# Optimization experiments

Measured on AMD Instinct MI355X. Metric: run time of the kernel, lower is better.

Reference implementation:

```python
import jax, jax.numpy as jnp
import numpy as np

NUM_REL = 20000
NUM_EDGES = 640000
DIM_IN = 128
DIM_OUT = 128
NUM_HEAD = 8
DIM_HID = DIM_OUT // NUM_HEAD
NUM_BIN = 10
NEG_SLOPE = 0.2


def leaky_relu(x):
    return jnp.where(x >= 0, x, NEG_SLOPE * x)


def setup_inputs() -> dict:
    key = jax.random.key(0)
    ks = jax.random.split(key, 8)
    emb_rel = jax.random.normal(ks[0], (NUM_REL, DIM_IN), dtype=jnp.float32)
    head = jax.random.randint(ks[1], (NUM_EDGES, 1), 0, NUM_REL)
    tail = jax.random.randint(ks[2], (NUM_EDGES, 1), 0, NUM_REL)
    bins = jax.random.randint(ks[3], (NUM_EDGES, 1), 0, NUM_BIN)
    relation_triplets = jnp.concatenate([head, tail, bins], axis=-1).astype(jnp.int64)
    # xavier-normal-ish init
    attn_proj_w = jax.random.normal(ks[4], (DIM_OUT, 2 * DIM_IN), dtype=jnp.float32) * (2.0 / np.sqrt(2 * DIM_IN + DIM_OUT))
    attn_proj_b = jnp.zeros((DIM_OUT,), dtype=jnp.float32)
    attn_bin = jax.random.normal(ks[5], (NUM_BIN, NUM_HEAD, 1), dtype=jnp.float32) * 0.3
    attn_vec = jax.random.normal(ks[6], (1, NUM_HEAD, DIM_HID), dtype=jnp.float32) * (2.0 / np.sqrt(NUM_HEAD * DIM_HID))
    aggr_proj_w = jax.random.normal(ks[7], (DIM_OUT, DIM_IN), dtype=jnp.float32) * (2.0 / np.sqrt(DIM_IN + DIM_OUT))
    aggr_proj_b = jnp.zeros((DIM_OUT,), dtype=jnp.float32)
    return {"emb_rel": emb_rel, "relation_triplets": relation_triplets,
            "attn_proj_w": attn_proj_w, "attn_proj_b": attn_proj_b,
            "attn_bin": attn_bin, "attn_vec": attn_vec,
            "aggr_proj_w": aggr_proj_w, "aggr_proj_b": aggr_proj_b}


def reference(emb_rel, relation_triplets, attn_proj_w, attn_proj_b, attn_bin, attn_vec, aggr_proj_w, aggr_proj_b):
    num_rel = emb_rel.shape[0]
    head = relation_triplets[..., 0]
    tail = relation_triplets[..., 1]
    bins = relation_triplets[..., 2]
    # edge gather + concat: [E, 2*dim_in]
    concat = jnp.concatenate([emb_rel[head], emb_rel[tail]], axis=-1)
    proj = concat @ attn_proj_w.T + attn_proj_b  # [E, dim_out]
    proj = leaky_relu(proj).reshape(-1, NUM_HEAD, DIM_HID)
    attn_raw = (proj * attn_vec).sum(axis=-1, keepdims=True) + leaky_relu(attn_bin[bins])  # [E,H,1]
    # per-head-relation segment softmax over edges grouped by head index
    seg_max = jax.ops.segment_max(attn_raw, head, num_segments=num_rel)  # [R,H,1]
    attn_val = jnp.exp(attn_raw - seg_max[head])
    seg_sum = jax.ops.segment_sum(attn_val, head, num_segments=num_rel)  # [R,H,1]
    beta = attn_val / (seg_sum[head] + 1e-16)
    msg = (emb_rel[tail] @ aggr_proj_w.T + aggr_proj_b).reshape(-1, NUM_HEAD, DIM_HID)
    out = jax.ops.segment_sum(beta * msg, head, num_segments=num_rel)  # [R,H,Dh]
    return out.reshape(num_rel, -1)
```

## Files before the change

kernel.cpp:

```cpp
#include <hip/hip_runtime.h>
#include <hip/hip_bf16.h>
#include <cstdint>
#include <cstddef>

#define NUM_REL    20000
#define NUM_EDGES  640000
#define DIM        128
#define NUM_HEAD   8
#define DIM_HID    16
#define NUM_BIN    10
#define CAP        128
#define PROJ_BLKS  471
#define SC_BLKS    2500

using u16 = unsigned short;
using u32 = unsigned int;
typedef __attribute__((ext_vector_type(8))) short bf16x8;
typedef __attribute__((ext_vector_type(4))) float f32x4;

__device__ __forceinline__ float b2f(u16 u) { return __uint_as_float(((u32)u) << 16); }
__device__ __forceinline__ float lo2f(u32 u) { return __uint_as_float(u << 16); }
__device__ __forceinline__ float hi2f(u32 u) { return __uint_as_float(u & 0xffff0000u); }
__device__ __forceinline__ float lrelu(float x) { return fmaxf(x, 0.2f * x); }
__device__ __forceinline__ int clampi(int v, int hi) { return v < 0 ? 0 : (v > hi ? hi : v); }
__device__ __forceinline__ float ldf(const void* p, int f32m, int i)
{ return f32m ? ((const float*)p)[i] : b2f(((const u16*)p)[i]); }
__device__ __forceinline__ u16 f2b(float x)
{ u32 u = __float_as_uint(x); u += 0x7fffu + ((u >> 16) & 1u); return (u16)(u >> 16); }
__device__ __forceinline__ u32 pk2(float a, float b)
{ return (u32)f2b(a) | ((u32)f2b(b) << 16); }

__device__ __forceinline__ void detect_flags(const int* __restrict__ trip,
                                             const u16* __restrict__ emb,
                                             int* sF, int tid)
{
    if (tid < 64) {
        bool odd_zero = (trip[2 * tid + 1] == 0) && (trip[2 * tid + 129] == 0);
        unsigned long long m1 = __ballot(odd_zero);
        int ex = (emb[2 * tid] >> 7) & 0xFF;
        bool inr = (ex >= 110) && (ex <= 136);
        unsigned long long m2 = __ballot(inr);
        if (tid == 0) {
            sF[0] = (~m1 == 0ull) ? 1 : 0;
            sF[1] = (__popcll(m2) >= 32) ? 0 : 1;
        }
    }
    __syncthreads();
}

__global__ __launch_bounds__(256) void k_projscatter(
    const void* __restrict__ emb, const int* __restrict__ trip,
    const void* __restrict__ w_attn, const void* __restrict__ w_aggr,
    const void* __restrict__ b_attn, const void* __restrict__ b_aggr,
    float* __restrict__ A, u16* __restrict__ Bb, u16* __restrict__ Mb,
    int* __restrict__ cnt, int* __restrict__ bucket)
{
    __shared__ u16 sA[128 * 128];
    __shared__ u16 sW[128 * 128];
    __shared__ float sBias[128];
    __shared__ int sF[2];

    const int tid = threadIdx.x;
    detect_flags(trip, (const u16*)emb, sF, tid);
    const int is64 = sF[0], f32m = sF[1];

    if (blockIdx.x >= PROJ_BLKS) {
        int e = (blockIdx.x - PROJ_BLKS) * 256 + tid;
        if (e < NUM_EDGES) {
            int h, t, b;
            if (is64) { h = trip[6 * e]; t = trip[6 * e + 2]; b = trip[6 * e + 4]; }
            else      { h = trip[3 * e]; t = trip[3 * e + 1]; b = trip[3 * e + 2]; }
            h = clampi(h, NUM_REL - 1);
            t = clampi(t, NUM_REL - 1);
            b = clampi(b, NUM_BIN - 1);
            int pos = atomicAdd(&cnt[h], 1);
            if (pos < CAP) bucket[h * CAP + pos] = t | (b << 20);
        }
        return;
    }

    const int mt = blockIdx.x / 3, nt = blockIdx.x % 3;
    const int r0 = mt * 128;

    if (tid < 128)
        sBias[tid] = (nt == 0) ? 0.f : ldf((nt == 1) ? b_attn : b_aggr, f32m, tid);

    if (f32m) {
        const float* src = (const float*)emb;
        #pragma unroll
        for (int i = 0; i < 16; ++i) {
            int f = i * 256 + tid;
            int row = f >> 5, pos = f & 31;
            int g = r0 + row;
            float4 x = (g < NUM_REL) ? ((const float4*)(src + (size_t)g * DIM))[pos]
                                     : make_float4(0.f, 0.f, 0.f, 0.f);
            int chunk = (pos >> 1) ^ (row & 15);
            *(uint2*)&sA[row * 128 + chunk * 8 + (pos & 1) * 4] =
                make_uint2(pk2(x.x, x.y), pk2(x.z, x.w));
        }
    } else {
        const u16* src = (const u16*)emb;
        #pragma unroll
        for (int i = 0; i < 8; ++i) {
            int f = i * 256 + tid;
            int row = f >> 4, pos = f & 15;
            int g = r0 + row;
            uint4 x = (g < NUM_REL) ? ((const uint4*)(src + (size_t)g * DIM))[pos]
                                    : make_uint4(0, 0, 0, 0);
            int chunk = pos ^ (row & 15);
            *(uint4*)&sA[row * 128 + chunk * 8] = x;
        }
    }

    {
        const void* wsrc = (nt == 2) ? w_aggr : w_attn;
        const int stride = (nt == 2) ? 128 : 256;
        const int koff   = (nt == 1) ? 128 : 0;
        if (f32m) {
            const float* src = (const float*)wsrc;
            #pragma unroll
            for (int i = 0; i < 16; ++i) {
                int f = i * 256 + tid;
                int row = f >> 5, pos = f & 31;
                float4 x = ((const float4*)(src + (size_t)row * stride + koff))[pos];
                int chunk = (pos >> 1) ^ (row & 15);
                *(uint2*)&sW[row * 128 + chunk * 8 + (pos & 1) * 4] =
                    make_uint2(pk2(x.x, x.y), pk2(x.z, x.w));
            }
        } else {
            const u16* src = (const u16*)wsrc;
            #pragma unroll
            for (int i = 0; i < 8; ++i) {
                int f = i * 256 + tid;
                int row = f >> 4, pos = f & 15;
                uint4 x = ((const uint4*)(src + (size_t)row * stride + koff))[pos];
                int chunk = pos ^ (row & 15);
                *(uint4*)&sW[row * 128 + chunk * 8] = x;
            }
        }
    }
    __syncthreads();

    const int lane = tid & 63, wid = tid >> 6;
    const int wm = (wid >> 1) * 64, wn = (wid & 1) * 64;
    const int ln15 = lane & 15, q = lane >> 4;

    f32x4 acc[4][4] = {};
    #pragma unroll
    for (int kk = 0; kk < 4; ++kk) {
        const int cbase = kk * 4 + q;
        bf16x8 a[4], b[4];
        #pragma unroll
        for (int mi = 0; mi < 4; ++mi) {
            int m = wm + mi * 16 + ln15;
            int c = cbase ^ ln15;
            a[mi] = *(const bf16x8*)&sA[m * 128 + c * 8];
        }
        #pragma unroll
        for (int ni = 0; ni < 4; ++ni) {
            int n = wn + ni * 16 + ln15;
            int c = cbase ^ ln15;
            b[ni] = *(const bf16x8*)&sW[n * 128 + c * 8];
        }
        #pragma unroll
        for (int mi = 0; mi < 4; ++mi)
            #pragma unroll
            for (int ni = 0; ni < 4; ++ni)
                acc[mi][ni] = __builtin_amdgcn_mfma_f32_16x16x32_bf16(
                    a[mi], b[ni], acc[mi][ni], 0, 0, 0);
    }

    #pragma unroll
    for (int mi = 0; mi < 4; ++mi) {
        #pragma unroll
        for (int reg = 0; reg < 4; ++reg) {
            int g = r0 + wm + mi * 16 + q * 4 + reg;
            if (g < NUM_REL) {
                #pragma unroll
                for (int ni = 0; ni < 4; ++ni) {
                    int c = wn + ni * 16 + ln15;
                    float v = acc[mi][ni][reg] + sBias[c];
                    size_t o = (size_t)g * DIM + c;
                    if (nt == 0)      A[o]  = v;
                    else if (nt == 1) Bb[o] = f2b(v);
                    else              Mb[o] = f2b(v);
                }
            }
        }
    }
}

__global__ __launch_bounds__(256, 6) void k_segment(
    const float* __restrict__ A, const u16* __restrict__ Bb,
    const u16* __restrict__ Mb, const void* __restrict__ attn_bin,
    const void* __restrict__ attn_vec, const int* __restrict__ cnt,
    const int* __restrict__ bucket, const int* __restrict__ trip,
    const void* __restrict__ emb, void* __restrict__ out)
{
    __shared__ float sAr[4][DIM];
    __shared__ float sVec[DIM];
    __shared__ float sBin[NUM_BIN * NUM_HEAD];
    __shared__ int sF[2];

    const int tid  = threadIdx.x;
    detect_flags(trip, (const u16*)emb, sF, tid);
    const int f32m = sF[1];

    const int wid  = tid >> 6, lane = tid & 63;
    const int r = blockIdx.x * 4 + wid;
    int nE = cnt[r]; if (nE > CAP) nE = CAP;
    const int* __restrict__ bk = bucket + r * CAP;

    {
        const float2* ap = (const float2*)(A + (size_t)r * DIM);
        float2 a2 = ap[lane];
        sAr[wid][2 * lane] = a2.x; sAr[wid][2 * lane + 1] = a2.y;
    }
    if (tid < DIM) sVec[tid] = ldf(attn_vec, f32m, tid);
    else if (tid < DIM + NUM_BIN * NUM_HEAD)
        sBin[tid - DIM] = lrelu(ldf(attn_bin, f32m, tid - DIM));
    __syncthreads();

    if (nE == 0) {
        if (f32m) ((float2*)out)[(size_t)r * 64 + lane] = make_float2(0.f, 0.f);
        else      ((u32*)out)[(size_t)r * 64 + lane] = 0;
        return;
    }

    const int el = lane >> 3, hd = lane & 7;
    const int ah = lane >> 3;

    float av[16], vv[16];
    {
        const float4* pA = (const float4*)(&sAr[wid][hd * DIM_HID]);
        const float4* pV = (const float4*)(&sVec[hd * DIM_HID]);
        #pragma unroll
        for (int i = 0; i < 4; ++i) {
            float4 a4 = pA[i], v4 = pV[i];
            av[4*i+0]=a4.x; av[4*i+1]=a4.y; av[4*i+2]=a4.z; av[4*i+3]=a4.w;
            vv[4*i+0]=v4.x; vv[4*i+1]=v4.y; vv[4*i+2]=v4.z; vv[4*i+3]=v4.w;
        }
    }

    float l = 0.f, accx = 0.f, accy = 0.f;

    bool act = el < nE;
    int tb = act ? bk[el] : 0;
    int t  = tb & 0xFFFFF;
    const uint4* Bt0p = (const uint4*)(Bb + (size_t)t * DIM) + hd * 2;
    uint4 q0 = Bt0p[0], q1 = Bt0p[1];

    for (int base = 0; base < nE; base += 8) {
        int e_n = base + 8 + el;
        bool act_n = e_n < nE;
        int tb_n = act_n ? bk[e_n] : 0;
        int t_n  = tb_n & 0xFFFFF;
        const uint4* Btn = (const uint4*)(Bb + (size_t)t_n * DIM) + hd * 2;
        uint4 q0n = Btn[0], q1n = Btn[1];

        float p = 0.f;
        {
            int b = (tb >> 20) & 0xF;
            float s = sBin[b * NUM_HEAD + hd];
            s += lrelu(av[0]  + lo2f(q0.x)) * vv[0];
            s += lrelu(av[1]  + hi2f(q0.x)) * vv[1];
            s += lrelu(av[2]  + lo2f(q0.y)) * vv[2];
            s += lrelu(av[3]  + hi2f(q0.y)) * vv[3];
            s += lrelu(av[4]  + lo2f(q0.z)) * vv[4];
            s += lrelu(av[5]  + hi2f(q0.z)) * vv[5];
            s += lrelu(av[6]  + lo2f(q0.w)) * vv[6];
            s += lrelu(av[7]  + hi2f(q0.w)) * vv[7];
            s += lrelu(av[8]  + lo2f(q1.x)) * vv[8];
            s += lrelu(av[9]  + hi2f(q1.x)) * vv[9];
            s += lrelu(av[10] + lo2f(q1.y)) * vv[10];
            s += lrelu(av[11] + hi2f(q1.y)) * vv[11];
            s += lrelu(av[12] + lo2f(q1.z)) * vv[12];
            s += lrelu(av[13] + hi2f(q1.z)) * vv[13];
            s += lrelu(av[14] + lo2f(q1.w)) * vv[14];
            s += lrelu(av[15] + hi2f(q1.w)) * vv[15];
            s = fminf(fmaxf(s, -60.f), 60.f);
            p = act ? __expf(s) : 0.f;
        }
        l += p;

        int lim = nE - base; if (lim > 8) lim = 8;
        #pragma unroll
        for (int k = 0; k < 8; ++k) {
            if (k < lim) {
                float v = __shfl(p, k * 8 + ah);
                int tk  = __shfl(t, k * 8);
                u32 mm = *(const u32*)(Mb + (size_t)tk * DIM + 2 * lane);
                accx += v * lo2f(mm);
                accy += v * hi2f(mm);
            }
        }

        act = act_n; tb = tb_n; t = t_n; q0 = q0n; q1 = q1n;
    }

    float lt = l + __shfl_xor(l, 8);
    lt += __shfl_xor(lt, 16);
    lt += __shfl_xor(lt, 32);
    float lA = __shfl(lt, ah);
    float inv = 1.0f / (lA + 1e-16f);
    float o0 = accx * inv, o1 = accy * inv;
    if (f32m) {
        ((float2*)out)[(size_t)r * 64 + lane] = make_float2(o0, o1);
    } else {
        u32 pk = (u32)f2b(o0) | ((u32)f2b(o1) << 16);
        ((u32*)out)[(size_t)r * 64 + lane] = pk;
    }
}

extern "C" void kernel_launch(void* const* d_in, const int* in_sizes, int n_in,
                              void* d_out, int out_size, void* d_ws, size_t ws_size,
                              hipStream_t stream)
{
    (void)in_sizes; (void)n_in; (void)out_size; (void)ws_size;
    const void* emb      = d_in[0];
    const int*  trip     = (const int*)d_in[1];
    const void* w_attn   = d_in[2];
    const void* b_attn   = d_in[3];
    const void* attn_bin = d_in[4];
    const void* attn_vec = d_in[5];
    const void* w_aggr   = d_in[6];
    const void* b_aggr   = d_in[7];

    char* p = (char*)d_ws;
    float* A      = (float*)p; p += (size_t)NUM_REL * DIM * 4;
    u16*   Bb     = (u16*)p;   p += (size_t)NUM_REL * DIM * 2;
    u16*   Mb     = (u16*)p;   p += (size_t)NUM_REL * DIM * 2;
    int*   bucket = (int*)p;   p += (size_t)NUM_REL * CAP * 4;
    int*   cnt    = (int*)p;   p += (size_t)NUM_REL * 4;

    hipMemsetAsync(cnt, 0, NUM_REL * sizeof(int), stream);
    k_projscatter<<<PROJ_BLKS + SC_BLKS, 256, 0, stream>>>(
        emb, trip, w_attn, w_aggr, b_attn, b_aggr, A, Bb, Mb, cnt, bucket);
    k_segment<<<NUM_REL / 4, 256, 0, stream>>>(A, Bb, Mb, attn_bin, attn_vec,
                                               cnt, bucket, trip, emb, d_out);
}
```

Baseline: 194.7 us.

## Interleave tail-projection layout per head and drop software prefetch in segment loop

The tail-projection buffer Bb is now stored head-interleaved, so the first 8 hidden dims of all heads form one contiguous 128-byte block and the last 8 form a second. Each lane then loads uint4 at hd and 8+hd, and the 8 head lanes of an edge read contiguous memory, which should coalesce better. The explicit next-iteration prefetch of bucket indices and Bb rows is removed, and those loads now happen inside the loop under an active guard. This cuts register pressure but may expose gather latency the prefetch used to hide.

```diff
diff --git a/kernel.cpp b/kernel.cpp
--- a/kernel.cpp
+++ b/kernel.cpp
@@ -180,10 +180,15 @@
                 for (int ni = 0; ni < 4; ++ni) {
                     int c = wn + ni * 16 + ln15;
                     float v = acc[mi][ni][reg] + sBias[c];
-                    size_t o = (size_t)g * DIM + c;
-                    if (nt == 0)      A[o]  = v;
-                    else if (nt == 1) Bb[o] = f2b(v);
-                    else              Mb[o] = f2b(v);
+                    if (nt == 0) {
+                        A[(size_t)g * DIM + c] = v;
+                    } else if (nt == 1) {
+                        int hd = c >> 4, d = c & 15;
+                        int pos = ((d >> 3) << 6) + hd * 8 + (d & 7);
+                        Bb[(size_t)g * DIM + pos] = f2b(v);
+                    } else {
+                        Mb[(size_t)g * DIM + c] = f2b(v);
+                    }
                 }
             }
         }
@@ -244,23 +249,18 @@
 
     float l = 0.f, accx = 0.f, accy = 0.f;
 
-    bool act = el < nE;
-    int tb = act ? bk[el] : 0;
-    int t  = tb & 0xFFFFF;
-    const uint4* Bt0p = (const uint4*)(Bb + (size_t)t * DIM) + hd * 2;
-    uint4 q0 = Bt0p[0], q1 = Bt0p[1];
-
     for (int base = 0; base < nE; base += 8) {
-        int e_n = base + 8 + el;
-        bool act_n = e_n < nE;
-        int tb_n = act_n ? bk[e_n] : 0;
-        int t_n  = tb_n & 0xFFFFF;
-        const uint4* Btn = (const uint4*)(Bb + (size_t)t_n * DIM) + hd * 2;
-        uint4 q0n = Btn[0], q1n = Btn[1];
-
+        int e = base + el;
+        bool act = e < nE;
+        int tb = 0;
+        if (act) tb = bk[e];
+        int t = tb & 0xFFFFF;
         float p = 0.f;
-        {
+        if (act) {
             int b = (tb >> 20) & 0xF;
+            const uint4* Bt = (const uint4*)(Bb + (size_t)t * DIM);
+            uint4 q0 = Bt[hd];
+            uint4 q1 = Bt[8 + hd];
             float s = sBin[b * NUM_HEAD + hd];
             s += lrelu(av[0]  + lo2f(q0.x)) * vv[0];
             s += lrelu(av[1]  + hi2f(q0.x)) * vv[1];
@@ -279,7 +279,7 @@
             s += lrelu(av[14] + lo2f(q1.w)) * vv[14];
             s += lrelu(av[15] + hi2f(q1.w)) * vv[15];
             s = fminf(fmaxf(s, -60.f), 60.f);
-            p = act ? __expf(s) : 0.f;
+            p = __expf(s);
         }
         l += p;
 
@@ -294,8 +294,6 @@
                 accy += v * hi2f(mm);
             }
         }
-
-        act = act_n; tb = tb_n; t = t_n; q0 = q0n; q1 = q1n;
     }
 
     float lt = l + __shfl_xor(l, 8);
```

After: 201.7 us. +3.6%, slower.
